# Kernel optimization log

Measured on AMD Instinct MI355X. Metric: run time of the kernel, lower is better.

## Reference

```python
import jax, jax.numpy as jnp
import numpy as np
import math

B, S, E_PHI, E_F, H_F, N_HEADS = 2, 2048, 1024, 1024, 1024, 16


def setup_inputs() -> dict:
    key = jax.random.key(0)
    ks = jax.random.split(key, 7)
    return {
        "q": jax.random.normal(ks[0], (B, S, E_PHI), dtype=jnp.float32),
        "k": jax.random.normal(ks[1], (B, S, E_PHI), dtype=jnp.float32),
        "v": jax.random.normal(ks[2], (B, S, E_F), dtype=jnp.float32),
        # weights stored as [in, out]; applied as x @ W (same math as nn.Linear with W^T)
        "W_q": jax.random.normal(ks[3], (E_PHI, H_F), dtype=jnp.float32) * 0.02,
        "W_k": jax.random.normal(ks[4], (E_PHI, H_F), dtype=jnp.float32) * 0.02,
        "W_v": jax.random.normal(ks[5], (E_F, H_F), dtype=jnp.float32) * 0.02,
        "W_o": jax.random.normal(ks[6], (H_F, E_F), dtype=jnp.float32) * 0.02,
    }


def reference(q, k, v, W_q, W_k, W_v, W_o):
    Bq, Sq, _ = q.shape
    Dh = H_F // N_HEADS
    scale = 1.0 / math.sqrt(H_F)
    # projections -> [B, H, S, Dh]
    qh = (q @ W_q).reshape(Bq, Sq, N_HEADS, Dh).transpose(0, 2, 1, 3)
    kh = (k @ W_k).reshape(Bq, Sq, N_HEADS, Dh).transpose(0, 2, 1, 3)
    vh = (v @ W_v).reshape(Bq, Sq, N_HEADS, Dh).transpose(0, 2, 1, 3)
    # near-causal mask: mask out j >= i (triu incl. diagonal), EXCEPT position [0,0]
    mask = jnp.triu(jnp.ones((Sq, Sq), dtype=bool), 0).at[0, 0].set(False)
    scores = jnp.einsum('bhsd,bhtd->bhst', qh, kh) * scale  # [B,H,S,S]
    scores = jnp.where(mask, -jnp.inf, scores)
    probs = jax.nn.softmax(scores, axis=-1)  # dropout = identity (eval mode)
    out = jnp.einsum('bhst,bhtd->bhsd', probs, vh)  # [B,H,S,Dh]
    out = out.transpose(0, 2, 1, 3).reshape(Bq, Sq, H_F)
    return out @ W_o
```

## Files before the change

### kernel.cpp

```cpp
#include <hip/hip_runtime.h>
#include <type_traits>

#define S_LEN 2048
#define NHEAD 16
#define DHEAD 64
#define EMB   1024
#define NBATCH 2

typedef __bf16 bf16_t;
typedef bf16_t bf16x8 __attribute__((ext_vector_type(8)));
typedef float  f32x4  __attribute__((ext_vector_type(4)));
typedef unsigned short us_t;
typedef us_t   us8    __attribute__((ext_vector_type(8)));
typedef us_t   us4    __attribute__((ext_vector_type(4)));
typedef unsigned int u32x4 __attribute__((ext_vector_type(4)));
typedef unsigned int u32x2 __attribute__((ext_vector_type(2)));
typedef short  s16x4  __attribute__((ext_vector_type(4)));

static __device__ __forceinline__ bf16x8 ld_bf16x8(const us_t* p) {
  return __builtin_bit_cast(bf16x8, *reinterpret_cast<const us8*>(p));
}
static __device__ __forceinline__ us_t f2bf(float f) {
  bf16_t h = (bf16_t)f;
  return __builtin_bit_cast(us_t, h);
}
static __device__ __forceinline__ void gload16(const void* g, void* lds) {
  __builtin_amdgcn_global_load_lds((const __attribute__((address_space(1))) void*)g,
                                   (__attribute__((address_space(3))) void*)lds,
                                   16, 0, 0);
}

__global__ __launch_bounds__(256) void cvt3(const float* __restrict__ A0,
                                            const float* __restrict__ A1,
                                            const float* __restrict__ A2,
                                            us_t* __restrict__ O0,
                                            us_t* __restrict__ O1,
                                            us_t* __restrict__ O2) {
  const int z = blockIdx.z;
  const float* A = (z == 0) ? A0 : (z == 1) ? A1 : A2;
  us_t* O = (z == 0) ? O0 : (z == 1) ? O1 : O2;
  const size_t i = ((size_t)blockIdx.x * 256 + threadIdx.x) * 8;
  f32x4 lo = *reinterpret_cast<const f32x4*>(A + i);
  f32x4 hi = *reinterpret_cast<const f32x4*>(A + i + 4);
  us8 w;
#pragma unroll
  for (int j = 0; j < 4; ++j) { w[j] = f2bf(lo[j]); w[j + 4] = f2bf(hi[j]); }
  *reinterpret_cast<us8*>(O + i) = w;
}

__global__ __launch_bounds__(256) void wtrans4(const float* __restrict__ W0,
                                               const float* __restrict__ W1,
                                               const float* __restrict__ W2,
                                               const float* __restrict__ W3,
                                               us_t* __restrict__ O0,
                                               us_t* __restrict__ O1,
                                               us_t* __restrict__ O2,
                                               us_t* __restrict__ O3) {
  __shared__ float tile[32][33];
  const int z = blockIdx.z;
  const float* W = (z == 0) ? W0 : (z == 1) ? W1 : (z == 2) ? W2 : W3;
  us_t* WT = (z == 0) ? O0 : (z == 1) ? O1 : (z == 2) ? O2 : O3;
  const int n0 = blockIdx.x * 32, k0 = blockIdx.y * 32;
  const int tx = threadIdx.x & 31, ty = threadIdx.x >> 5;
#pragma unroll
  for (int i = 0; i < 32; i += 8)
    tile[ty + i][tx] = W[(size_t)(k0 + ty + i) * EMB + n0 + tx];
  __syncthreads();
#pragma unroll
  for (int i = 0; i < 32; i += 8)
    WT[(size_t)(n0 + ty + i) * EMB + k0 + tx] = f2bf(tile[tx][ty + i]);
}

template<int MODE>
static __device__ __forceinline__ void gemm_core(const us_t* __restrict__ A,
                                                 const us_t* __restrict__ BT,
                                                 void* __restrict__ O,
                                                 int mt, int nt,
                                                 char (*As)[8192], char (*Bs)[8192]) {
  const int lane = threadIdx.x & 63;
  const int wave = threadIdx.x >> 6;
  const int wm = (wave >> 1) * 64;
  const int wn = (wave & 1) * 64;
  const int lr = lane & 15;
  const int lg = lane >> 4;

  f32x4 acc[4][4] = {};

  auto stage = [&](int buf, int k0) {
#pragma unroll
    for (int i = 0; i < 2; ++i) {
      const int seg = wave * 2 + i;
      const int r = seg * 16 + (lane >> 2);
      const int cb = (lane & 3) * 16;
      gload16((const char*)A + ((size_t)(mt * 128 + r) * EMB + k0) * 2 + cb,
              &As[buf][seg * 1024]);
      gload16((const char*)BT + ((size_t)(nt * 128 + r) * EMB + k0) * 2 + cb,
              &Bs[buf][seg * 1024]);
    }
  };

  stage(0, 0);
  __syncthreads();

  for (int ks = 0; ks < EMB / 32; ++ks) {
    const int cur = ks & 1;
    if (ks + 1 < EMB / 32) stage(cur ^ 1, (ks + 1) * 32);
    bf16x8 af[4], bfr[4];
#pragma unroll
    for (int i = 0; i < 4; ++i)
      af[i] = ld_bf16x8((const us_t*)&As[cur][(wm + 16 * i + lr) * 64 + lg * 16]);
#pragma unroll
    for (int j = 0; j < 4; ++j)
      bfr[j] = ld_bf16x8((const us_t*)&Bs[cur][(wn + 16 * j + lr) * 64 + lg * 16]);
#pragma unroll
    for (int i = 0; i < 4; ++i)
#pragma unroll
      for (int j = 0; j < 4; ++j)
        acc[i][j] = __builtin_amdgcn_mfma_f32_16x16x32_bf16(af[i], bfr[j], acc[i][j], 0, 0, 0);
    __syncthreads();
  }

  const int crow = (lane >> 4) * 4;
#pragma unroll
  for (int i = 0; i < 4; ++i)
#pragma unroll
    for (int j = 0; j < 4; ++j)
#pragma unroll
      for (int r = 0; r < 4; ++r) {
        const int m = mt * 128 + wm + 16 * i + crow + r;
        const int n = nt * 128 + wn + 16 * j + lr;
        const float val = acc[i][j][r];
        if constexpr (MODE == 2) {
          ((float*)O)[(size_t)m * EMB + n] = val;
        } else {
          us_t* o = (us_t*)O;
          const int b = m >> 11, s = m & (S_LEN - 1);
          const int h = n >> 6, d = n & 63;
          if constexpr (MODE == 0)
            o[(((size_t)(b * NHEAD + h) * S_LEN + s) << 6) + d] = f2bf(val);
          else
            o[((size_t)(b * NHEAD + h) * DHEAD + d) * S_LEN + s] = f2bf(val);
        }
      }
}

__global__ __launch_bounds__(256) void proj3(const us_t* __restrict__ A0,
                                             const us_t* __restrict__ A1,
                                             const us_t* __restrict__ A2,
                                             const us_t* __restrict__ B0,
                                             const us_t* __restrict__ B1,
                                             const us_t* __restrict__ B2,
                                             us_t* __restrict__ O0,
                                             us_t* __restrict__ O1,
                                             us_t* __restrict__ O2) {
  __shared__ char As[2][8192];
  __shared__ char Bs[2][8192];
  const int f = blockIdx.x;
  const int w = (f & 7) * 96 + (f >> 3);
  const int z = w >> 8;
  const int rem = w & 255;
  const int mt = rem >> 3, nt = rem & 7;
  const us_t* A = (z == 0) ? A0 : (z == 1) ? A1 : A2;
  const us_t* BT = (z == 0) ? B0 : (z == 1) ? B1 : B2;
  us_t* O = (z == 0) ? O0 : (z == 1) ? O1 : O2;
  if (z < 2)
    gemm_core<0>(A, BT, O, mt, nt, As, Bs);
  else
    gemm_core<1>(A, BT, O, mt, nt, As, Bs);
}

__global__ __launch_bounds__(256) void gemmout(const us_t* __restrict__ A,
                                               const us_t* __restrict__ BT,
                                               float* __restrict__ O) {
  __shared__ char As[2][8192];
  __shared__ char Bs[2][8192];
  const int f = blockIdx.x;
  const int w = (f & 7) * 32 + (f >> 3);
  const int mt = w >> 3, nt = w & 7;
  gemm_core<2>(A, BT, O, mt, nt, As, Bs);
}

__global__ __launch_bounds__(256, 4) void attn64(const us_t* __restrict__ Qh,
                                                 const us_t* __restrict__ Kh,
                                                 const us_t* __restrict__ Vt,
                                                 us_t* __restrict__ AO) {
  __shared__ char Ks[2][8192];
  __shared__ char Vs[2][8192];
  const int flat = blockIdx.y * 32 + blockIdx.x;
  const int bh = (flat & 7) * 4 + ((flat >> 3) & 3);
  const int qt = 31 - (flat >> 5);
  const int lane = threadIdx.x & 63;
  const int wave = threadIdx.x >> 6;
  const int lr = lane & 15;
  const int lg = lane >> 4;
  const int q_glob = qt * 64 + wave * 16 + lr;

  const us_t* qbase = Qh + ((size_t)bh * S_LEN + q_glob) * DHEAD;
  bf16x8 qf[2] = { ld_bf16x8(qbase + lg * 8), ld_bf16x8(qbase + 32 + lg * 8) };

  const us_t* kbase0 = Kh + (size_t)bh * S_LEN * DHEAD;
  const us_t* vbase0 = Vt + (size_t)bh * DHEAD * S_LEN;

  auto stage = [&](int buf, int t0) {
#pragma unroll
    for (int i = 0; i < 2; ++i) {
      const int seg = wave * 2 + i;
      const int r = seg * 8 + (lane >> 3);
      const int c16 = (lane & 7) ^ (lane >> 3);
      gload16(kbase0 + (size_t)(t0 + r) * DHEAD + c16 * 8, &Ks[buf][seg * 1024]);
      gload16(vbase0 + (size_t)r * S_LEN + t0 + c16 * 8, &Vs[buf][seg * 1024]);
    }
  };

  f32x4 oaccT[4] = {};
  float mrow = -1e9f;
  float lsum = 0.f;
  const float c = 0.045084220f;

  stage(0, 0);
  __syncthreads();

  for (int tt = 0; tt <= qt; ++tt) {
    const int cur = tt & 1;
    if (tt < qt) stage(cur ^ 1, (tt + 1) * 64);

    f32x4 sc[4] = {};
#pragma unroll
    for (int ks = 0; ks < 2; ++ks)
#pragma unroll
      for (int j = 0; j < 4; ++j) {
        bf16x8 ak = ld_bf16x8((const us_t*)&Ks[cur][(16 * j + lr) * 128 +
                              ((ks * 64 + lg * 16) ^ ((lr & 7) << 4))]);
        sc[j] = __builtin_amdgcn_mfma_f32_16x16x32_bf16(ak, qf[ks], sc[j], 0, 0, 0);
      }

    if (tt == qt) {
#pragma unroll
      for (int j = 0; j < 4; ++j)
#pragma unroll
        for (int r = 0; r < 4; ++r) {
          const int t_g = tt * 64 + 16 * j + 4 * lg + r;
          if (!((t_g < q_glob) || (q_glob == 0 && t_g == 0))) sc[j][r] = -1e30f;
        }
    }

    float mx = sc[0][0];
#pragma unroll
    for (int j = 0; j < 4; ++j)
#pragma unroll
      for (int r = 0; r < 4; ++r) mx = fmaxf(mx, sc[j][r]);
    const float mxc = mx * c;
    if (__any(mxc > mrow + 8.f)) {
      float mc = mxc;
      mc = fmaxf(mc, __shfl_xor(mc, 16, 64));
      mc = fmaxf(mc, __shfl_xor(mc, 32, 64));
      const float m2 = fmaxf(mrow, mc);
      const float alpha = exp2f(mrow - m2);
      lsum *= alpha;
#pragma unroll
      for (int j = 0; j < 4; ++j)
#pragma unroll
        for (int r = 0; r < 4; ++r) oaccT[j][r] *= alpha;
      mrow = m2;
    }

    unsigned int pk[4][2];
    float ps = 0.f;
#pragma unroll
    for (int j = 0; j < 4; ++j) {
      float p0 = exp2f(__builtin_fmaf(sc[j][0], c, -mrow));
      float p1 = exp2f(__builtin_fmaf(sc[j][1], c, -mrow));
      float p2 = exp2f(__builtin_fmaf(sc[j][2], c, -mrow));
      float p3 = exp2f(__builtin_fmaf(sc[j][3], c, -mrow));
      ps += (p0 + p1) + (p2 + p3);
      pk[j][0] = (unsigned)f2bf(p0) | ((unsigned)f2bf(p1) << 16);
      pk[j][1] = (unsigned)f2bf(p2) | ((unsigned)f2bf(p3) << 16);
    }
    lsum += ps;

#if __has_builtin(__builtin_amdgcn_mfma_f32_16x16x16bf16_1k)
#pragma unroll
    for (int jk = 0; jk < 4; ++jk) {
      s16x4 pf = __builtin_bit_cast(s16x4, (u32x2){pk[jk][0], pk[jk][1]});
#pragma unroll
      for (int jd = 0; jd < 4; ++jd) {
        const int addr = (16 * jd + lr) * 128 + ((32 * jk + 8 * lg) ^ ((lr & 7) << 4));
        s16x4 av = __builtin_bit_cast(s16x4, *reinterpret_cast<const us4*>(&Vs[cur][addr]));
        oaccT[jd] = __builtin_amdgcn_mfma_f32_16x16x16bf16_1k(av, pf, oaccT[jd], 0, 0, 0);
      }
    }
#else
    {
      const int srcA = (2 * (lg & 1)) * 16 + lr;
      const int srcB = srcA + 16;
      const bool hi = (lg >> 1) != 0;
      u32x4 bw[2];
#pragma unroll
      for (int ks = 0; ks < 2; ++ks) {
        unsigned a0 = __shfl((int)pk[2 * ks][0], srcA, 64);
        unsigned a0b = __shfl((int)pk[2 * ks + 1][0], srcA, 64);
        unsigned a1 = __shfl((int)pk[2 * ks][1], srcA, 64);
        unsigned a1b = __shfl((int)pk[2 * ks + 1][1], srcA, 64);
        unsigned b0 = __shfl((int)pk[2 * ks][0], srcB, 64);
        unsigned b0b = __shfl((int)pk[2 * ks + 1][0], srcB, 64);
        unsigned b1 = __shfl((int)pk[2 * ks][1], srcB, 64);
        unsigned b1b = __shfl((int)pk[2 * ks + 1][1], srcB, 64);
        bw[ks][0] = hi ? a0b : a0;
        bw[ks][1] = hi ? a1b : a1;
        bw[ks][2] = hi ? b0b : b0;
        bw[ks][3] = hi ? b1b : b1;
      }
#pragma unroll
      for (int ks = 0; ks < 2; ++ks) {
        bf16x8 pf = __builtin_bit_cast(bf16x8, bw[ks]);
#pragma unroll
        for (int j = 0; j < 4; ++j) {
          bf16x8 av = ld_bf16x8((const us_t*)&Vs[cur][(16 * j + lr) * 128 +
                                ((ks * 64 + lg * 16) ^ ((lr & 7) << 4))]);
          oaccT[j] = __builtin_amdgcn_mfma_f32_16x16x32_bf16(av, pf, oaccT[j], 0, 0, 0);
        }
      }
    }
#endif
    __syncthreads();
  }

  lsum += __shfl_xor(lsum, 16, 64);
  lsum += __shfl_xor(lsum, 32, 64);
  const float inv = 1.0f / lsum;
  const int b = bh >> 4, h = bh & 15;
  us_t* aout = AO + (size_t)(b * S_LEN + q_glob) * EMB + h * DHEAD;
#pragma unroll
  for (int j = 0; j < 4; ++j) {
    us4 w;
#pragma unroll
    for (int r = 0; r < 4; ++r) w[r] = f2bf(oaccT[j][r] * inv);
    *reinterpret_cast<us4*>(aout + 16 * j + 4 * lg) = w;
  }
}

extern "C" void kernel_launch(void* const* d_in, const int* in_sizes, int n_in,
                              void* d_out, int out_size, void* d_ws, size_t ws_size,
                              hipStream_t stream) {
  const float* q  = (const float*)d_in[0];
  const float* k  = (const float*)d_in[1];
  const float* v  = (const float*)d_in[2];
  const float* Wq = (const float*)d_in[3];
  const float* Wk = (const float*)d_in[4];
  const float* Wv = (const float*)d_in[5];
  const float* Wo = (const float*)d_in[6];
  float* out = (float*)d_out;

  char* ws = (char*)d_ws;
  const size_t MB = 1024 * 1024;
  us_t* WqT = (us_t*)(ws + 0 * MB);
  us_t* WkT = (us_t*)(ws + 2 * MB);
  us_t* WvT = (us_t*)(ws + 4 * MB);
  us_t* WoT = (us_t*)(ws + 6 * MB);
  us_t* Qh  = (us_t*)(ws + 8 * MB);
  us_t* Kh  = (us_t*)(ws + 16 * MB);
  us_t* Vt  = (us_t*)(ws + 24 * MB);
  us_t* AO  = (us_t*)(ws + 32 * MB);
  us_t* Qb  = (us_t*)(ws + 32 * MB);
  us_t* Kb  = (us_t*)(ws + 40 * MB);
  us_t* Vb  = (us_t*)(ws + 48 * MB);

  cvt3<<<dim3((NBATCH * S_LEN * EMB) / (256 * 8), 1, 3), 256, 0, stream>>>(
      q, k, v, Qb, Kb, Vb);
  wtrans4<<<dim3(EMB / 32, EMB / 32, 4), 256, 0, stream>>>(Wq, Wk, Wv, Wo,
                                                           WqT, WkT, WvT, WoT);

  proj3<<<768, 256, 0, stream>>>(Qb, Kb, Vb, WqT, WkT, WvT, Qh, Kh, Vt);

  attn64<<<dim3(S_LEN / 64, NBATCH * NHEAD), 256, 0, stream>>>(Qh, Kh, Vt, AO);

  gemmout<<<256, 256, 0, stream>>>(AO, WoT, out);
}
```

Before: 134.7 us.

## Merge conversion kernels and micro-optimize attention inner loop

Merges the input conversion and weight transpose kernels into a single prep launch with a 7-slice grid, which saves one kernel launch. In the attention kernel it precomputes the swizzled LDS offsets for K and V, raises wave priority around the MFMA blocks, uses the hardware exp2 builtin, and packs bf16 pairs with v_cvt_pk_bf16_f32. It also drops the fallback shuffle path, so the kernel now requires the 16x16x16 bf16 MFMA builtin. The precomputed offsets need 24 more registers, which may reduce occupancy, and the prep grid launches weight blocks that exit immediately.

```diff
diff --git a/kernel.cpp b/kernel.cpp
--- a/kernel.cpp
+++ b/kernel.cpp
@@ -24,51 +24,64 @@
   bf16_t h = (bf16_t)f;
   return __builtin_bit_cast(us_t, h);
 }
+static __device__ __forceinline__ unsigned cvt_pk_bf16(float lo, float hi) {
+  unsigned r;
+  asm("v_cvt_pk_bf16_f32 %0, %1, %2" : "=v"(r) : "v"(lo), "v"(hi));
+  return r;
+}
+#if __has_builtin(__builtin_amdgcn_exp2f)
+#define EXP2(x) __builtin_amdgcn_exp2f(x)
+#else
+#define EXP2(x) exp2f(x)
+#endif
 static __device__ __forceinline__ void gload16(const void* g, void* lds) {
   __builtin_amdgcn_global_load_lds((const __attribute__((address_space(1))) void*)g,
                                    (__attribute__((address_space(3))) void*)lds,
                                    16, 0, 0);
 }
 
-__global__ __launch_bounds__(256) void cvt3(const float* __restrict__ A0,
-                                            const float* __restrict__ A1,
-                                            const float* __restrict__ A2,
-                                            us_t* __restrict__ O0,
-                                            us_t* __restrict__ O1,
-                                            us_t* __restrict__ O2) {
+__global__ __launch_bounds__(256) void prep(const float* __restrict__ q,
+                                            const float* __restrict__ k,
+                                            const float* __restrict__ v,
+                                            const float* __restrict__ W0,
+                                            const float* __restrict__ W1,
+                                            const float* __restrict__ W2,
+                                            const float* __restrict__ W3,
+                                            us_t* __restrict__ Qb,
+                                            us_t* __restrict__ Kb,
+                                            us_t* __restrict__ Vb,
+                                            us_t* __restrict__ T0,
+                                            us_t* __restrict__ T1,
+                                            us_t* __restrict__ T2,
+                                            us_t* __restrict__ T3) {
   const int z = blockIdx.z;
-  const float* A = (z == 0) ? A0 : (z == 1) ? A1 : A2;
-  us_t* O = (z == 0) ? O0 : (z == 1) ? O1 : O2;
-  const size_t i = ((size_t)blockIdx.x * 256 + threadIdx.x) * 8;
-  f32x4 lo = *reinterpret_cast<const f32x4*>(A + i);
-  f32x4 hi = *reinterpret_cast<const f32x4*>(A + i + 4);
-  us8 w;
-#pragma unroll
-  for (int j = 0; j < 4; ++j) { w[j] = f2bf(lo[j]); w[j + 4] = f2bf(hi[j]); }
-  *reinterpret_cast<us8*>(O + i) = w;
-}
-
-__global__ __launch_bounds__(256) void wtrans4(const float* __restrict__ W0,
-                                               const float* __restrict__ W1,
-                                               const float* __restrict__ W2,
-                                               const float* __restrict__ W3,
-                                               us_t* __restrict__ O0,
-                                               us_t* __restrict__ O1,
-                                               us_t* __restrict__ O2,
-                                               us_t* __restrict__ O3) {
-  __shared__ float tile[32][33];
-  const int z = blockIdx.z;
-  const float* W = (z == 0) ? W0 : (z == 1) ? W1 : (z == 2) ? W2 : W3;
-  us_t* WT = (z == 0) ? O0 : (z == 1) ? O1 : (z == 2) ? O2 : O3;
-  const int n0 = blockIdx.x * 32, k0 = blockIdx.y * 32;
-  const int tx = threadIdx.x & 31, ty = threadIdx.x >> 5;
-#pragma unroll
-  for (int i = 0; i < 32; i += 8)
-    tile[ty + i][tx] = W[(size_t)(k0 + ty + i) * EMB + n0 + tx];
-  __syncthreads();
-#pragma unroll
-  for (int i = 0; i < 32; i += 8)
-    WT[(size_t)(n0 + ty + i) * EMB + k0 + tx] = f2bf(tile[tx][ty + i]);
+  if (z < 3) {
+    const float* A = (z == 0) ? q : (z == 1) ? k : v;
+    us_t* O = (z == 0) ? Qb : (z == 1) ? Kb : Vb;
+    const int flat = blockIdx.y * 32 + blockIdx.x;
+    const size_t i = ((size_t)flat * 256 + threadIdx.x) * 8;
+    f32x4 lo = *reinterpret_cast<const f32x4*>(A + i);
+    f32x4 hi = *reinterpret_cast<const f32x4*>(A + i + 4);
+    us8 w;
+#pragma unroll
+    for (int j = 0; j < 4; ++j) { w[j] = f2bf(lo[j]); w[j + 4] = f2bf(hi[j]); }
+    *reinterpret_cast<us8*>(O + i) = w;
+  } else {
+    if (blockIdx.y >= EMB / 32) return;
+    __shared__ float tile[32][33];
+    const int zz = z - 3;
+    const float* W = (zz == 0) ? W0 : (zz == 1) ? W1 : (zz == 2) ? W2 : W3;
+    us_t* WT = (zz == 0) ? T0 : (zz == 1) ? T1 : (zz == 2) ? T2 : T3;
+    const int n0 = blockIdx.x * 32, k0 = blockIdx.y * 32;
+    const int tx = threadIdx.x & 31, ty = threadIdx.x >> 5;
+#pragma unroll
+    for (int i = 0; i < 32; i += 8)
+      tile[ty + i][tx] = W[(size_t)(k0 + ty + i) * EMB + n0 + tx];
+    __syncthreads();
+#pragma unroll
+    for (int i = 0; i < 32; i += 8)
+      WT[(size_t)(n0 + ty + i) * EMB + k0 + tx] = f2bf(tile[tx][ty + i]);
+  }
 }
 
 template<int MODE>
@@ -201,6 +214,19 @@
   const us_t* kbase0 = Kh + (size_t)bh * S_LEN * DHEAD;
   const us_t* vbase0 = Vt + (size_t)bh * DHEAD * S_LEN;
 
+  int koff[8];
+#pragma unroll
+  for (int ks = 0; ks < 2; ++ks)
+#pragma unroll
+    for (int j = 0; j < 4; ++j)
+      koff[ks * 4 + j] = (16 * j + lr) * 128 + ((ks * 64 + lg * 16) ^ ((lr & 7) << 4));
+  int voff[16];
+#pragma unroll
+  for (int jk = 0; jk < 4; ++jk)
+#pragma unroll
+    for (int jd = 0; jd < 4; ++jd)
+      voff[jk * 4 + jd] = (16 * jd + lr) * 128 + ((32 * jk + 8 * lg) ^ ((lr & 7) << 4));
+
   auto stage = [&](int buf, int t0) {
 #pragma unroll
     for (int i = 0; i < 2; ++i) {
@@ -225,14 +251,15 @@
     if (tt < qt) stage(cur ^ 1, (tt + 1) * 64);
 
     f32x4 sc[4] = {};
+    __builtin_amdgcn_s_setprio(1);
 #pragma unroll
     for (int ks = 0; ks < 2; ++ks)
 #pragma unroll
       for (int j = 0; j < 4; ++j) {
-        bf16x8 ak = ld_bf16x8((const us_t*)&Ks[cur][(16 * j + lr) * 128 +
-                              ((ks * 64 + lg * 16) ^ ((lr & 7) << 4))]);
+        bf16x8 ak = ld_bf16x8((const us_t*)&Ks[cur][koff[ks * 4 + j]]);
         sc[j] = __builtin_amdgcn_mfma_f32_16x16x32_bf16(ak, qf[ks], sc[j], 0, 0, 0);
       }
+    __builtin_amdgcn_s_setprio(0);
 
     if (tt == qt) {
 #pragma unroll
@@ -255,7 +282,7 @@
       mc = fmaxf(mc, __shfl_xor(mc, 16, 64));
       mc = fmaxf(mc, __shfl_xor(mc, 32, 64));
       const float m2 = fmaxf(mrow, mc);
-      const float alpha = exp2f(mrow - m2);
+      const float alpha = EXP2(mrow - m2);
       lsum *= alpha;
 #pragma unroll
       for (int j = 0; j < 4; ++j)
@@ -268,60 +295,28 @@
     float ps = 0.f;
 #pragma unroll
     for (int j = 0; j < 4; ++j) {
-      float p0 = exp2f(__builtin_fmaf(sc[j][0], c, -mrow));
-      float p1 = exp2f(__builtin_fmaf(sc[j][1], c, -mrow));
-      float p2 = exp2f(__builtin_fmaf(sc[j][2], c, -mrow));
-      float p3 = exp2f(__builtin_fmaf(sc[j][3], c, -mrow));
+      float p0 = EXP2(__builtin_fmaf(sc[j][0], c, -mrow));
+      float p1 = EXP2(__builtin_fmaf(sc[j][1], c, -mrow));
+      float p2 = EXP2(__builtin_fmaf(sc[j][2], c, -mrow));
+      float p3 = EXP2(__builtin_fmaf(sc[j][3], c, -mrow));
       ps += (p0 + p1) + (p2 + p3);
-      pk[j][0] = (unsigned)f2bf(p0) | ((unsigned)f2bf(p1) << 16);
-      pk[j][1] = (unsigned)f2bf(p2) | ((unsigned)f2bf(p3) << 16);
+      pk[j][0] = cvt_pk_bf16(p0, p1);
+      pk[j][1] = cvt_pk_bf16(p2, p3);
     }
     lsum += ps;
 
-#if __has_builtin(__builtin_amdgcn_mfma_f32_16x16x16bf16_1k)
+    __builtin_amdgcn_s_setprio(1);
 #pragma unroll
     for (int jk = 0; jk < 4; ++jk) {
       s16x4 pf = __builtin_bit_cast(s16x4, (u32x2){pk[jk][0], pk[jk][1]});
 #pragma unroll
       for (int jd = 0; jd < 4; ++jd) {
-        const int addr = (16 * jd + lr) * 128 + ((32 * jk + 8 * lg) ^ ((lr & 7) << 4));
-        s16x4 av = __builtin_bit_cast(s16x4, *reinterpret_cast<const us4*>(&Vs[cur][addr]));
+        s16x4 av = __builtin_bit_cast(s16x4,
+            *reinterpret_cast<const us4*>(&Vs[cur][voff[jk * 4 + jd]]));
         oaccT[jd] = __builtin_amdgcn_mfma_f32_16x16x16bf16_1k(av, pf, oaccT[jd], 0, 0, 0);
       }
     }
-#else
-    {
-      const int srcA = (2 * (lg & 1)) * 16 + lr;
-      const int srcB = srcA + 16;
-      const bool hi = (lg >> 1) != 0;
-      u32x4 bw[2];
-#pragma unroll
-      for (int ks = 0; ks < 2; ++ks) {
-        unsigned a0 = __shfl((int)pk[2 * ks][0], srcA, 64);
-        unsigned a0b = __shfl((int)pk[2 * ks + 1][0], srcA, 64);
-        unsigned a1 = __shfl((int)pk[2 * ks][1], srcA, 64);
-        unsigned a1b = __shfl((int)pk[2 * ks + 1][1], srcA, 64);
-        unsigned b0 = __shfl((int)pk[2 * ks][0], srcB, 64);
-        unsigned b0b = __shfl((int)pk[2 * ks + 1][0], srcB, 64);
-        unsigned b1 = __shfl((int)pk[2 * ks][1], srcB, 64);
-        unsigned b1b = __shfl((int)pk[2 * ks + 1][1], srcB, 64);
-        bw[ks][0] = hi ? a0b : a0;
-        bw[ks][1] = hi ? a1b : a1;
-        bw[ks][2] = hi ? b0b : b0;
-        bw[ks][3] = hi ? b1b : b1;
-      }
-#pragma unroll
-      for (int ks = 0; ks < 2; ++ks) {
-        bf16x8 pf = __builtin_bit_cast(bf16x8, bw[ks]);
-#pragma unroll
-        for (int j = 0; j < 4; ++j) {
-          bf16x8 av = ld_bf16x8((const us_t*)&Vs[cur][(16 * j + lr) * 128 +
-                                ((ks * 64 + lg * 16) ^ ((lr & 7) << 4))]);
-          oaccT[j] = __builtin_amdgcn_mfma_f32_16x16x32_bf16(av, pf, oaccT[j], 0, 0, 0);
-        }
-      }
-    }
-#endif
+    __builtin_amdgcn_s_setprio(0);
     __syncthreads();
   }
 
@@ -365,10 +360,8 @@
   us_t* Kb  = (us_t*)(ws + 40 * MB);
   us_t* Vb  = (us_t*)(ws + 48 * MB);
 
-  cvt3<<<dim3((NBATCH * S_LEN * EMB) / (256 * 8), 1, 3), 256, 0, stream>>>(
-      q, k, v, Qb, Kb, Vb);
-  wtrans4<<<dim3(EMB / 32, EMB / 32, 4), 256, 0, stream>>>(Wq, Wk, Wv, Wo,
-                                                           WqT, WkT, WvT, WoT);
+  prep<<<dim3(32, 64, 7), 256, 0, stream>>>(q, k, v, Wq, Wk, Wv, Wo,
+                                            Qb, Kb, Vb, WqT, WkT, WvT, WoT);
 
   proj3<<<768, 256, 0, stream>>>(Qb, Kb, Vb, WqT, WkT, WvT, Qh, Kh, Vt);
 
```

Result: faster. 130.6 us (-3.1%).
